# Kernel optimization log

Measured on AMD Instinct MI355X. Metric: run time of the kernel, lower is better.

The kernel has to match this reference:

```python
import jax, jax.numpy as jnp
import numpy as np

N, K, F_IN, F_OUT, P = 50000, 32, 64, 64, 3


def setup_inputs() -> dict:
    key = jax.random.key(0)
    k1, k2, k3, k4, k5 = jax.random.split(key, 5)
    h = jax.random.normal(k1, (N, F_IN), dtype=jnp.float32)
    pos = jax.random.normal(k2, (N, P), dtype=jnp.float32)
    neighbor_idx = jax.random.randint(k3, (N, K), 0, N, dtype=jnp.int32)
    weight = jax.random.normal(k4, (K * F_IN, F_OUT), dtype=jnp.float32) * 0.02
    bias_p = jax.random.normal(k5, (1, F_OUT), dtype=jnp.float32) * 0.02
    return {"h": h, "pos": pos, "neighbor_idx": neighbor_idx,
            "weight": weight, "bias_p": bias_p}


def reference(h, pos, neighbor_idx, weight, bias_p):
    n, k = neighbor_idx.shape
    msgs = h[neighbor_idx]                      # [N, K, F_IN] gather
    diff = pos[:, None, :] - pos[neighbor_idx]  # [N, K, P]
    sq = jnp.sum(diff * diff, axis=2, keepdims=True)  # [N, K, 1]
    # torch: dist[dist==0] = 0.5 ; safe-sqrt avoids NaN grads at 0
    dist = jnp.where(sq == 0.0, 0.5, jnp.sqrt(jnp.where(sq == 0.0, 1.0, sq)))
    wow = (msgs / dist).reshape(n, k * h.shape[1])  # [N, K*F_IN]
    h1 = wow @ weight + bias_p                   # [N, F_OUT]
    return jax.nn.leaky_relu(h1, negative_slope=0.01)
```

## Files before the change

kernel.cpp:

```cpp
#include <hip/hip_runtime.h>


#define N_NODES 50000
#define KN      32
#define FIN     64
#define FOUT    64
#define MTILE   64

typedef __attribute__((ext_vector_type(4))) float    f32x4;
typedef __attribute__((ext_vector_type(8))) _Float16 f16x8;
typedef __attribute__((ext_vector_type(4))) _Float16 f16x4;

__global__ void k_prep(const float* __restrict__ w, _Float16* __restrict__ wf,
                       const float* __restrict__ h, _Float16* __restrict__ hb) {
    __shared__ float s_w[32 * 64];
    const int tid = threadIdx.x;
    if (blockIdx.x < 64) {
        const int kk = blockIdx.x;
        for (int p = tid; p < 32 * 64; p += 256)
            s_w[p] = w[kk * 32 * 64 + p];
        __syncthreads();
        const int t = tid >> 6, lane = tid & 63;
        const int lm = lane & 15, q = lane >> 4;
        f16x8 o;
        #pragma unroll
        for (int i = 0; i < 8; ++i)
            o[i] = (_Float16)s_w[(q * 8 + i) * 64 + t * 16 + lm];
        *(f16x8*)(wf + kk * 2048 + t * 512 + lane * 8) = o;
    } else {
        const int i = (blockIdx.x - 64) * 256 + tid;
        float4 v = ((const float4*)h)[i];
        f16x4 o = { (_Float16)v.x, (_Float16)v.y, (_Float16)v.z, (_Float16)v.w };
        ((f16x4*)hb)[i] = o;
    }
}

__global__ __launch_bounds__(256, 4) void k_main(
        const _Float16* __restrict__ hf,
        const float*    __restrict__ pos,
        const int*      __restrict__ nidx,
        const _Float16* __restrict__ wf,
        const float*    __restrict__ bias,
        float*          __restrict__ out)
{
    __shared__ __align__(16) char smem[2 * 64 * 68 * 4];
    int2*  s_e   = (int2*)smem;
    float* s_red = (float*)smem;

    const int tid = threadIdx.x;
    const int m0  = blockIdx.x * MTILE;

    for (int p = tid; p < MTILE * KN; p += 256) {
        int m = p & 63, k = p >> 6;
        int node = m0 + m;
        int idx = 0; float scl = 0.f;
        if (node < N_NODES) {
            idx = nidx[node * KN + k];
            float dx = pos[node * 3 + 0] - pos[idx * 3 + 0];
            float dy = pos[node * 3 + 1] - pos[idx * 3 + 1];
            float dz = pos[node * 3 + 2] - pos[idx * 3 + 2];
            float sq = dx * dx + dy * dy + dz * dz;
            scl = (sq == 0.f) ? 2.0f : rsqrtf(sq);
        }
        s_e[k * MTILE + m] = make_int2(idx, __float_as_int(scl));
    }
    __syncthreads();

    const int lane = tid & 63, kg = tid >> 6;
    const int lm = lane & 15, q = lane >> 4;

    const _Float16* pb = wf + lane * 8;

    f32x4 acc[4][4] = {};

    #pragma unroll 1
    for (int j = 0; j < 8; ++j) {
        const int kn = kg * 8 + j;
        int2 e0 = s_e[kn * MTILE + lm];
        int2 e1 = s_e[kn * MTILE + 16 + lm];
        int2 e2 = s_e[kn * MTILE + 32 + lm];
        int2 e3 = s_e[kn * MTILE + 48 + lm];
        const _Float16* pa0 = hf + e0.x * FIN + q * 8;
        const _Float16* pa1 = hf + e1.x * FIN + q * 8;
        const _Float16* pa2 = hf + e2.x * FIN + q * 8;
        const _Float16* pa3 = hf + e3.x * FIN + q * 8;
        const _Float16 s0 = (_Float16)__int_as_float(e0.y);
        const _Float16 s1 = (_Float16)__int_as_float(e1.y);
        const _Float16 s2 = (_Float16)__int_as_float(e2.y);
        const _Float16 s3 = (_Float16)__int_as_float(e3.y);

        #pragma unroll
        for (int jh = 0; jh < 2; ++jh) {
            const _Float16* pbb = pb + (kn * 2 + jh) * 2048;
            f16x8 b0 = *(const f16x8*)(pbb);
            f16x8 b1 = *(const f16x8*)(pbb + 512);
            f16x8 b2 = *(const f16x8*)(pbb + 1024);
            f16x8 b3 = *(const f16x8*)(pbb + 1536);
            f16x8 a0 = *(const f16x8*)(pa0 + jh * 32) * s0;
            f16x8 a1 = *(const f16x8*)(pa1 + jh * 32) * s1;
            f16x8 a2 = *(const f16x8*)(pa2 + jh * 32) * s2;
            f16x8 a3 = *(const f16x8*)(pa3 + jh * 32) * s3;
            acc[0][0] = __builtin_amdgcn_mfma_f32_16x16x32_f16(a0, b0, acc[0][0], 0, 0, 0);
            acc[0][1] = __builtin_amdgcn_mfma_f32_16x16x32_f16(a0, b1, acc[0][1], 0, 0, 0);
            acc[0][2] = __builtin_amdgcn_mfma_f32_16x16x32_f16(a0, b2, acc[0][2], 0, 0, 0);
            acc[0][3] = __builtin_amdgcn_mfma_f32_16x16x32_f16(a0, b3, acc[0][3], 0, 0, 0);
            acc[1][0] = __builtin_amdgcn_mfma_f32_16x16x32_f16(a1, b0, acc[1][0], 0, 0, 0);
            acc[1][1] = __builtin_amdgcn_mfma_f32_16x16x32_f16(a1, b1, acc[1][1], 0, 0, 0);
            acc[1][2] = __builtin_amdgcn_mfma_f32_16x16x32_f16(a1, b2, acc[1][2], 0, 0, 0);
            acc[1][3] = __builtin_amdgcn_mfma_f32_16x16x32_f16(a1, b3, acc[1][3], 0, 0, 0);
            acc[2][0] = __builtin_amdgcn_mfma_f32_16x16x32_f16(a2, b0, acc[2][0], 0, 0, 0);
            acc[2][1] = __builtin_amdgcn_mfma_f32_16x16x32_f16(a2, b1, acc[2][1], 0, 0, 0);
            acc[2][2] = __builtin_amdgcn_mfma_f32_16x16x32_f16(a2, b2, acc[2][2], 0, 0, 0);
            acc[2][3] = __builtin_amdgcn_mfma_f32_16x16x32_f16(a2, b3, acc[2][3], 0, 0, 0);
            acc[3][0] = __builtin_amdgcn_mfma_f32_16x16x32_f16(a3, b0, acc[3][0], 0, 0, 0);
            acc[3][1] = __builtin_amdgcn_mfma_f32_16x16x32_f16(a3, b1, acc[3][1], 0, 0, 0);
            acc[3][2] = __builtin_amdgcn_mfma_f32_16x16x32_f16(a3, b2, acc[3][2], 0, 0, 0);
            acc[3][3] = __builtin_amdgcn_mfma_f32_16x16x32_f16(a3, b3, acc[3][3], 0, 0, 0);
        }
    }

    __syncthreads();

    float* reg = s_red + (kg & 1) * (64 * 68);
    if (kg < 2) {
        #pragma unroll
        for (int mt = 0; mt < 4; ++mt)
            #pragma unroll
            for (int t = 0; t < 4; ++t)
                #pragma unroll
                for (int r = 0; r < 4; ++r)
                    reg[(mt * 16 + q * 4 + r) * 68 + t * 16 + lm] = acc[mt][t][r];
    }
    __syncthreads();
    if (kg >= 2) {
        #pragma unroll
        for (int mt = 0; mt < 4; ++mt)
            #pragma unroll
            for (int t = 0; t < 4; ++t)
                #pragma unroll
                for (int r = 0; r < 4; ++r)
                    reg[(mt * 16 + q * 4 + r) * 68 + t * 16 + lm] += acc[mt][t][r];
    }
    __syncthreads();

    const int row = tid >> 2, c0 = (tid & 3) * 16;
    const int node = m0 + row;
    if (node < N_NODES) {
        #pragma unroll
        for (int i = 0; i < 4; ++i) {
            int c = c0 + i * 4;
            f32x4 v0 = *(const f32x4*)(s_red + row * 68 + c);
            f32x4 v1 = *(const f32x4*)(s_red + 64 * 68 + row * 68 + c);
            f32x4 bb = *(const f32x4*)(bias + c);
            f32x4 o = v0 + v1 + bb;
            #pragma unroll
            for (int jj = 0; jj < 4; ++jj) o[jj] = o[jj] > 0.f ? o[jj] : 0.01f * o[jj];
            *(f32x4*)(out + node * FOUT + c) = o;
        }
    }
}

extern "C" void kernel_launch(void* const* d_in, const int* in_sizes, int n_in,
                              void* d_out, int out_size, void* d_ws, size_t ws_size,
                              hipStream_t stream) {
    const float* h    = (const float*)d_in[0];
    const float* pos  = (const float*)d_in[1];
    const int*   nidx = (const int*)d_in[2];
    const float* w    = (const float*)d_in[3];
    const float* bias = (const float*)d_in[4];
    float* out = (float*)d_out;

    _Float16* wf = (_Float16*)d_ws;
    _Float16* hb = (_Float16*)((char*)d_ws + 262144);

    k_prep<<<64 + (N_NODES * FIN / 4) / 256, 256, 0, stream>>>(w, wf, h, hb);
    k_main<<<(N_NODES + MTILE - 1) / MTILE, 256, 0, stream>>>(hb, pos, nidx, wf, bias, out);
}
```

Before: 128.9 us.

## Quantize node features to int8 with per-row scale for gather

Node features are quantized per row to offset int8 with a scale stored alongside the position in a packed float4. The main kernel gathers 16 bytes per lane instead of 32 and rebuilds fp16 values with an exponent-bias bit trick before the MFMA. This is meant to halve the gather traffic, which dominates cost, at the price of extra ALU work and reduced accuracy. The weight prep layout is reorganised to match the new per-lane K ordering.

```diff
diff --git a/kernel.cpp b/kernel.cpp
--- a/kernel.cpp
+++ b/kernel.cpp
@@ -9,39 +9,76 @@
 
 typedef __attribute__((ext_vector_type(4))) float    f32x4;
 typedef __attribute__((ext_vector_type(8))) _Float16 f16x8;
-typedef __attribute__((ext_vector_type(4))) _Float16 f16x4;
+
+static __device__ __forceinline__ f16x8 dec8i(unsigned int x, unsigned int y) {
+    union { unsigned int w[4]; f16x8 v; } r;
+    unsigned int xh = x >> 16, yh = y >> 16;
+    r.w[0] = 0x64006400u | ((x  & 0xFFu) << 2) | ((x  & 0xFF00u) << 10);
+    r.w[1] = 0x64006400u | ((xh & 0xFFu) << 2) | ((xh & 0xFF00u) << 10);
+    r.w[2] = 0x64006400u | ((y  & 0xFFu) << 2) | ((y  & 0xFF00u) << 10);
+    r.w[3] = 0x64006400u | ((yh & 0xFFu) << 2) | ((yh & 0xFF00u) << 10);
+    return r.v;
+}
 
 __global__ void k_prep(const float* __restrict__ w, _Float16* __restrict__ wf,
-                       const float* __restrict__ h, _Float16* __restrict__ hb) {
-    __shared__ float s_w[32 * 64];
+                       const float* __restrict__ h, unsigned char* __restrict__ hq,
+                       const float* __restrict__ pos, float4* __restrict__ posx) {
+    __shared__ float s_w[64 * 64];
     const int tid = threadIdx.x;
-    if (blockIdx.x < 64) {
-        const int kk = blockIdx.x;
-        for (int p = tid; p < 32 * 64; p += 256)
-            s_w[p] = w[kk * 32 * 64 + p];
+    if (blockIdx.x < 32) {
+        const int kn = blockIdx.x;
+        for (int p = tid; p < 64 * 64; p += 256)
+            s_w[p] = w[kn * 64 * 64 + p];
         __syncthreads();
         const int t = tid >> 6, lane = tid & 63;
         const int lm = lane & 15, q = lane >> 4;
-        f16x8 o;
-        #pragma unroll
-        for (int i = 0; i < 8; ++i)
-            o[i] = (_Float16)s_w[(q * 8 + i) * 64 + t * 16 + lm];
-        *(f16x8*)(wf + kk * 2048 + t * 512 + lane * 8) = o;
+        #pragma unroll
+        for (int jh = 0; jh < 2; ++jh) {
+            f16x8 o;
+            #pragma unroll
+            for (int i = 0; i < 8; ++i)
+                o[i] = (_Float16)s_w[(q * 16 + jh * 8 + i) * 64 + t * 16 + lm];
+            *(f16x8*)(wf + ((kn * 2 + jh) * 4 + t) * 512 + lane * 8) = o;
+        }
     } else {
-        const int i = (blockIdx.x - 64) * 256 + tid;
-        float4 v = ((const float4*)h)[i];
-        f16x4 o = { (_Float16)v.x, (_Float16)v.y, (_Float16)v.z, (_Float16)v.w };
-        ((f16x4*)hb)[i] = o;
+        const int r = (blockIdx.x - 32) * 256 + tid;
+        if (r < N_NODES) {
+            const float* hr = h + (size_t)r * FIN;
+            float v[64];
+            float amax = 0.f;
+            #pragma unroll
+            for (int i = 0; i < 16; ++i) {
+                float4 t4 = ((const float4*)hr)[i];
+                v[i * 4 + 0] = t4.x; v[i * 4 + 1] = t4.y;
+                v[i * 4 + 2] = t4.z; v[i * 4 + 3] = t4.w;
+                amax = fmaxf(amax, fmaxf(fmaxf(fabsf(t4.x), fabsf(t4.y)),
+                                         fmaxf(fabsf(t4.z), fabsf(t4.w))));
+            }
+            float scale = fmaxf(amax, 1e-30f) * (1.0f / 126.0f);
+            float inv = 126.0f / fmaxf(amax, 1e-30f);
+            union { unsigned char c[64]; uint4 u4[4]; } o;
+            #pragma unroll
+            for (int i = 0; i < 64; ++i) {
+                int q8 = __float2int_rn(v[i] * inv);
+                o.c[i] = (unsigned char)(q8 + 128);
+            }
+            uint4* dst = (uint4*)(hq + (size_t)r * 64);
+            dst[0] = o.u4[0]; dst[1] = o.u4[1]; dst[2] = o.u4[2]; dst[3] = o.u4[3];
+            float4 px;
+            px.x = pos[r * 3 + 0]; px.y = pos[r * 3 + 1]; px.z = pos[r * 3 + 2];
+            px.w = scale;
+            posx[r] = px;
+        }
     }
 }
 
 __global__ __launch_bounds__(256, 4) void k_main(
-        const _Float16* __restrict__ hf,
-        const float*    __restrict__ pos,
-        const int*      __restrict__ nidx,
-        const _Float16* __restrict__ wf,
-        const float*    __restrict__ bias,
-        float*          __restrict__ out)
+        const unsigned char* __restrict__ hq,
+        const float4*        __restrict__ posx,
+        const int*           __restrict__ nidx,
+        const _Float16*      __restrict__ wf,
+        const float*         __restrict__ bias,
+        float*               __restrict__ out)
 {
     __shared__ __align__(16) char smem[2 * 64 * 68 * 4];
     int2*  s_e   = (int2*)smem;
@@ -53,16 +90,17 @@
     for (int p = tid; p < MTILE * KN; p += 256) {
         int m = p & 63, k = p >> 6;
         int node = m0 + m;
-        int idx = 0; float scl = 0.f;
+        int idx = 0; float c1 = 0.f;
         if (node < N_NODES) {
             idx = nidx[node * KN + k];
-            float dx = pos[node * 3 + 0] - pos[idx * 3 + 0];
-            float dy = pos[node * 3 + 1] - pos[idx * 3 + 1];
-            float dz = pos[node * 3 + 2] - pos[idx * 3 + 2];
+            float4 pn = posx[node];
+            float4 pi = posx[idx];
+            float dx = pn.x - pi.x, dy = pn.y - pi.y, dz = pn.z - pi.z;
             float sq = dx * dx + dy * dy + dz * dz;
-            scl = (sq == 0.f) ? 2.0f : rsqrtf(sq);
-        }
-        s_e[k * MTILE + m] = make_int2(idx, __float_as_int(scl));
+            float scl = (sq == 0.f) ? 2.0f : rsqrtf(sq);
+            c1 = pi.w * scl * 0.25f;
+        }
+        s_e[k * MTILE + m] = make_int2(idx, __float_as_int(c1));
     }
     __syncthreads();
 
@@ -80,26 +118,26 @@
         int2 e1 = s_e[kn * MTILE + 16 + lm];
         int2 e2 = s_e[kn * MTILE + 32 + lm];
         int2 e3 = s_e[kn * MTILE + 48 + lm];
-        const _Float16* pa0 = hf + e0.x * FIN + q * 8;
-        const _Float16* pa1 = hf + e1.x * FIN + q * 8;
-        const _Float16* pa2 = hf + e2.x * FIN + q * 8;
-        const _Float16* pa3 = hf + e3.x * FIN + q * 8;
-        const _Float16 s0 = (_Float16)__int_as_float(e0.y);
-        const _Float16 s1 = (_Float16)__int_as_float(e1.y);
-        const _Float16 s2 = (_Float16)__int_as_float(e2.y);
-        const _Float16 s3 = (_Float16)__int_as_float(e3.y);
-
-        #pragma unroll
-        for (int jh = 0; jh < 2; ++jh) {
-            const _Float16* pbb = pb + (kn * 2 + jh) * 2048;
+        uint4 d0 = *(const uint4*)(hq + (size_t)e0.x * 64 + q * 16);
+        uint4 d1 = *(const uint4*)(hq + (size_t)e1.x * 64 + q * 16);
+        uint4 d2 = *(const uint4*)(hq + (size_t)e2.x * 64 + q * 16);
+        uint4 d3 = *(const uint4*)(hq + (size_t)e3.x * 64 + q * 16);
+        const _Float16 c0 = (_Float16)__int_as_float(e0.y);
+        const _Float16 c1 = (_Float16)__int_as_float(e1.y);
+        const _Float16 c2 = (_Float16)__int_as_float(e2.y);
+        const _Float16 c3 = (_Float16)__int_as_float(e3.y);
+        const _Float16 K = (_Float16)1536.0f;
+
+        {
+            const _Float16* pbb = pb + (kn * 2 + 0) * 2048;
             f16x8 b0 = *(const f16x8*)(pbb);
             f16x8 b1 = *(const f16x8*)(pbb + 512);
             f16x8 b2 = *(const f16x8*)(pbb + 1024);
             f16x8 b3 = *(const f16x8*)(pbb + 1536);
-            f16x8 a0 = *(const f16x8*)(pa0 + jh * 32) * s0;
-            f16x8 a1 = *(const f16x8*)(pa1 + jh * 32) * s1;
-            f16x8 a2 = *(const f16x8*)(pa2 + jh * 32) * s2;
-            f16x8 a3 = *(const f16x8*)(pa3 + jh * 32) * s3;
+            f16x8 a0 = (dec8i(d0.x, d0.y) - K) * c0;
+            f16x8 a1 = (dec8i(d1.x, d1.y) - K) * c1;
+            f16x8 a2 = (dec8i(d2.x, d2.y) - K) * c2;
+            f16x8 a3 = (dec8i(d3.x, d3.y) - K) * c3;
             acc[0][0] = __builtin_amdgcn_mfma_f32_16x16x32_f16(a0, b0, acc[0][0], 0, 0, 0);
             acc[0][1] = __builtin_amdgcn_mfma_f32_16x16x32_f16(a0, b1, acc[0][1], 0, 0, 0);
             acc[0][2] = __builtin_amdgcn_mfma_f32_16x16x32_f16(a0, b2, acc[0][2], 0, 0, 0);
@@ -117,6 +155,33 @@
             acc[3][2] = __builtin_amdgcn_mfma_f32_16x16x32_f16(a3, b2, acc[3][2], 0, 0, 0);
             acc[3][3] = __builtin_amdgcn_mfma_f32_16x16x32_f16(a3, b3, acc[3][3], 0, 0, 0);
         }
+        {
+            const _Float16* pbb = pb + (kn * 2 + 1) * 2048;
+            f16x8 b0 = *(const f16x8*)(pbb);
+            f16x8 b1 = *(const f16x8*)(pbb + 512);
+            f16x8 b2 = *(const f16x8*)(pbb + 1024);
+            f16x8 b3 = *(const f16x8*)(pbb + 1536);
+            f16x8 a0 = (dec8i(d0.z, d0.w) - K) * c0;
+            f16x8 a1 = (dec8i(d1.z, d1.w) - K) * c1;
+            f16x8 a2 = (dec8i(d2.z, d2.w) - K) * c2;
+            f16x8 a3 = (dec8i(d3.z, d3.w) - K) * c3;
+            acc[0][0] = __builtin_amdgcn_mfma_f32_16x16x32_f16(a0, b0, acc[0][0], 0, 0, 0);
+            acc[0][1] = __builtin_amdgcn_mfma_f32_16x16x32_f16(a0, b1, acc[0][1], 0, 0, 0);
+            acc[0][2] = __builtin_amdgcn_mfma_f32_16x16x32_f16(a0, b2, acc[0][2], 0, 0, 0);
+            acc[0][3] = __builtin_amdgcn_mfma_f32_16x16x32_f16(a0, b3, acc[0][3], 0, 0, 0);
+            acc[1][0] = __builtin_amdgcn_mfma_f32_16x16x32_f16(a1, b0, acc[1][0], 0, 0, 0);
+            acc[1][1] = __builtin_amdgcn_mfma_f32_16x16x32_f16(a1, b1, acc[1][1], 0, 0, 0);
+            acc[1][2] = __builtin_amdgcn_mfma_f32_16x16x32_f16(a1, b2, acc[1][2], 0, 0, 0);
+            acc[1][3] = __builtin_amdgcn_mfma_f32_16x16x32_f16(a1, b3, acc[1][3], 0, 0, 0);
+            acc[2][0] = __builtin_amdgcn_mfma_f32_16x16x32_f16(a2, b0, acc[2][0], 0, 0, 0);
+            acc[2][1] = __builtin_amdgcn_mfma_f32_16x16x32_f16(a2, b1, acc[2][1], 0, 0, 0);
+            acc[2][2] = __builtin_amdgcn_mfma_f32_16x16x32_f16(a2, b2, acc[2][2], 0, 0, 0);
+            acc[2][3] = __builtin_amdgcn_mfma_f32_16x16x32_f16(a2, b3, acc[2][3], 0, 0, 0);
+            acc[3][0] = __builtin_amdgcn_mfma_f32_16x16x32_f16(a3, b0, acc[3][0], 0, 0, 0);
+            acc[3][1] = __builtin_amdgcn_mfma_f32_16x16x32_f16(a3, b1, acc[3][1], 0, 0, 0);
+            acc[3][2] = __builtin_amdgcn_mfma_f32_16x16x32_f16(a3, b2, acc[3][2], 0, 0, 0);
+            acc[3][3] = __builtin_amdgcn_mfma_f32_16x16x32_f16(a3, b3, acc[3][3], 0, 0, 0);
+        }
     }
 
     __syncthreads();
@@ -143,12 +208,12 @@
     }
     __syncthreads();
 
-    const int row = tid >> 2, c0 = (tid & 3) * 16;
+    const int row = tid >> 2, c0e = (tid & 3) * 16;
     const int node = m0 + row;
     if (node < N_NODES) {
         #pragma unroll
         for (int i = 0; i < 4; ++i) {
-            int c = c0 + i * 4;
+            int c = c0e + i * 4;
             f32x4 v0 = *(const f32x4*)(s_red + row * 68 + c);
             f32x4 v1 = *(const f32x4*)(s_red + 64 * 68 + row * 68 + c);
             f32x4 bb = *(const f32x4*)(bias + c);
@@ -170,9 +235,11 @@
     const float* bias = (const float*)d_in[4];
     float* out = (float*)d_out;
 
-    _Float16* wf = (_Float16*)d_ws;
-    _Float16* hb = (_Float16*)((char*)d_ws + 262144);
-
-    k_prep<<<64 + (N_NODES * FIN / 4) / 256, 256, 0, stream>>>(w, wf, h, hb);
-    k_main<<<(N_NODES + MTILE - 1) / MTILE, 256, 0, stream>>>(hb, pos, nidx, wf, bias, out);
-}
+    _Float16*      wf   = (_Float16*)d_ws;
+    unsigned char* hq   = (unsigned char*)d_ws + 262144;
+    float4*        posx = (float4*)((char*)d_ws + 262144 + 3200000);
+
+    const int h_blocks = (N_NODES + 255) / 256;
+    k_prep<<<32 + h_blocks, 256, 0, stream>>>(w, wf, h, hq, pos, posx);
+    k_main<<<(N_NODES + MTILE - 1) / MTILE, 256, 0, stream>>>(hq, posx, nidx, wf, bias, out);
+}
```

Measured after the change: 115.5 us. 10.4% less time.
